# Performance work log

Measured on AMD Instinct MI355X. Metric: run time of the kernel, lower is better.

The kernel has to match this reference:

```python
import jax, jax.numpy as jnp
import numpy as np

B, T, D = 8, 2048, 256  # batch, time segments, feature dim (a_dim=v_dim=hidden=out=256)
EPS = 1e-8


def _layer_norm(x, g, b, eps=1e-6):
    m = jnp.mean(x, axis=-1, keepdims=True)
    v = jnp.var(x, axis=-1, keepdims=True)
    return (x - m) * jax.lax.rsqrt(v + eps) * g + b


def setup_inputs() -> dict:
    key = jax.random.key(0)
    ks = jax.random.split(key, 9)
    xav = lambda k: jax.random.uniform(k, (D, D), jnp.float32, -1.0, 1.0) * np.sqrt(6.0 / (D + D))
    return {
        "a_fea": jax.random.normal(ks[0], (B, T, D), jnp.float32),
        "v_fea": jax.random.normal(ks[1], (B, T, D), jnp.float32),
        "thr_val": jnp.float32(0.099),
        "Wv1": xav(ks[2]), "Wv2": xav(ks[3]), "Wvfc": xav(ks[4]),
        "Wa1": xav(ks[5]), "Wa2": xav(ks[6]), "Wafc": xav(ks[7]),
        "ln_g": jnp.ones((D,), jnp.float32),
        "ln_b": jnp.zeros((D,), jnp.float32),
    }


def reference(a_fea, v_fea, thr_val, Wv1, Wv2, Wvfc, Wa1, Wa2, Wafc, ln_g, ln_b):
    relu = jax.nn.relu
    # branch projections (dropout is identity at eval); torch Linear: x @ W.T
    v1 = relu(jnp.einsum('btd,hd->bth', v_fea, Wv1))
    v2 = relu(jnp.einsum('btd,hd->bth', v_fea, Wv2))
    a1 = relu(jnp.einsum('btd,hd->bth', a_fea, Wa1))
    a2 = relu(jnp.einsum('btd,hd->bth', a_fea, Wa2))

    d = v2.shape[-1]
    # scaled cross-modal scores, ReLU'd  [B, Tv, Ta]
    beta_va = relu(jnp.einsum('btd,bsd->bts', v2, a1) / jnp.sqrt(jnp.float32(d)))
    # a->v scores taken BEFORE row-normalization of beta_va (as in torch code)
    beta_av = jnp.transpose(beta_va, (0, 2, 1))

    time = beta_va.shape[-1]
    thr = thr_val * 10.0 / time

    # normalize -> threshold sparsify -> renormalize (v attends to a)
    bn_va = beta_va / (jnp.sum(beta_va, axis=-1, keepdims=True) + EPS)
    g_va = jnp.where(bn_va > thr, bn_va, 0.0)
    g_va = g_va / (jnp.sum(g_va, axis=-1, keepdims=True) + EPS)

    # same for a attends to v
    bn_av = beta_av / (jnp.sum(beta_av, axis=-1, keepdims=True) + EPS)
    g_av = jnp.where(bn_av > thr, bn_av, 0.0)
    g_av = g_av / (jnp.sum(g_av, axis=-1, keepdims=True) + EPS)

    # vectorized form of the diagonal selection double-loop (batch element 0)
    pred = (jnp.diagonal(g_av[0]) > 0).astype(jnp.float32)  # [T]

    a_pos = jnp.einsum('bts,bsd->btd', g_va, a2)
    v_psp = v_fea + a_pos
    v_pos = jnp.einsum('bts,bsd->btd', g_av, v1)
    a_psp = a_fea + v_pos

    v_psp = _layer_norm(relu(jnp.einsum('btd,od->bto', v_psp, Wvfc)), ln_g, ln_b)
    a_psp = _layer_norm(relu(jnp.einsum('btd,od->bto', a_psp, Wafc)), ln_g, ln_b)
    a_v_fuse = 0.5 * (v_psp + a_psp)
    return a_v_fuse, v_psp, a_psp, pred
```

## Files before the change

kernel.cpp:

```cpp
#include <hip/hip_runtime.h>
#include <math.h>

#define TT 2048
#define DD 256
#define NBATCH 8
#define EPSF 1e-8f

typedef unsigned short u16;
typedef __attribute__((ext_vector_type(8))) short short8;
typedef __attribute__((ext_vector_type(4))) float f32x4;

__device__ __forceinline__ u16 f2bf(float x) {
    unsigned int u = __builtin_bit_cast(unsigned int, x);
    u += 0x7fffu + ((u >> 16) & 1u);
    return (u16)(u >> 16);
}
__device__ __forceinline__ float bf2f(u16 h) {
    return __builtin_bit_cast(float, (unsigned int)h << 16);
}

__device__ __forceinline__ int frag_dst(int row, int k) {
    return (((row >> 4) * 4 + (k >> 3)) * 16 + (row & 15)) * 8 + (k & 7);
}

__device__ __forceinline__ int swz(int i) { return i ^ ((i >> 2) & 32); }

template<int BR>
__device__ __forceinline__ void stage_tile(const u16* __restrict__ g, u16* s,
                                           int row0, int k0, int ldk, int tid)
{
    #pragma unroll
    for (int i = 0; i < BR / 64; ++i) {
        const int c = tid + 256 * i;
        const int row = c >> 2, q = c & 3;
        *(int4*)(s + swz(frag_dst(row, q * 8))) =
            *(const int4*)(g + (long)(row0 + row) * ldk + k0 + q * 8);
    }
}

__global__ __launch_bounds__(256)
void proj_kernel(const u16* __restrict__ vfh, const u16* __restrict__ vfl,
                 const u16* __restrict__ afh, const u16* __restrict__ afl,
                 const u16* __restrict__ Wsp,
                 u16* __restrict__ v2h, u16* __restrict__ v2l,
                 u16* __restrict__ a1h, u16* __restrict__ a1l,
                 u16* __restrict__ v1T, u16* __restrict__ a2T)
{
    const int zz = blockIdx.z;
    const u16* Ah = (zz == 1 || zz == 3) ? afh : vfh;
    const u16* Al = (zz == 1 || zz == 3) ? afl : vfl;
    const int widx = (zz == 0) ? 2 : (zz == 1) ? 4 : (zz == 2) ? 0 : 6;
    const u16* Bh = Wsp + widx * DD * DD;
    const u16* Bl = Bh + DD * DD;
    const bool split = zz < 2;
    u16* Oh = (zz == 0) ? v2h : a1h;
    u16* Ol = (zz == 0) ? v2l : a1l;
    u16* OT = (zz == 2) ? v1T : a2T;

    __shared__ __align__(16) u16 Ah_s[64 * 32], Al_s[64 * 32];
    __shared__ __align__(16) u16 Bh_s[64 * 32], Bl_s[64 * 32];
    const int m0 = blockIdx.y * 64, n0 = blockIdx.x * 64;
    const int tid = threadIdx.x, lane = tid & 63, w = tid >> 6;
    const int wy = w >> 1, wx = w & 1;
    f32x4 acc[2][2] = {};

    for (int k0 = 0; k0 < DD; k0 += 32) {
        stage_tile<64>(Ah, Ah_s, m0, k0, DD, tid);
        stage_tile<64>(Al, Al_s, m0, k0, DD, tid);
        stage_tile<64>(Bh, Bh_s, n0, k0, DD, tid);
        stage_tile<64>(Bl, Bl_s, n0, k0, DD, tid);
        __syncthreads();
        short8 ah[2], al[2], bh[2], bl[2];
        #pragma unroll
        for (int i = 0; i < 2; ++i) {
            ah[i] = *(const short8*)(Ah_s + swz(((wy * 2 + i) * 64 + lane) * 8));
            al[i] = *(const short8*)(Al_s + swz(((wy * 2 + i) * 64 + lane) * 8));
        }
        #pragma unroll
        for (int j = 0; j < 2; ++j) {
            bh[j] = *(const short8*)(Bh_s + swz(((wx * 2 + j) * 64 + lane) * 8));
            bl[j] = *(const short8*)(Bl_s + swz(((wx * 2 + j) * 64 + lane) * 8));
        }
        #pragma unroll
        for (int i = 0; i < 2; ++i)
            #pragma unroll
            for (int j = 0; j < 2; ++j) {
                acc[i][j] = __builtin_amdgcn_mfma_f32_16x16x32_bf16(ah[i], bl[j], acc[i][j], 0, 0, 0);
                acc[i][j] = __builtin_amdgcn_mfma_f32_16x16x32_bf16(al[i], bh[j], acc[i][j], 0, 0, 0);
                acc[i][j] = __builtin_amdgcn_mfma_f32_16x16x32_bf16(ah[i], bh[j], acc[i][j], 0, 0, 0);
            }
        __syncthreads();
    }
    const int quad = lane >> 4, col = lane & 15;
    #pragma unroll
    for (int i = 0; i < 2; ++i)
        #pragma unroll
        for (int j = 0; j < 2; ++j) {
            const int c = n0 + (wx * 2 + j) * 16 + col;
            const int rbase = m0 + (wy * 2 + i) * 16 + quad * 4;
            if (split) {
                #pragma unroll
                for (int r = 0; r < 4; ++r) {
                    const float v = fmaxf(acc[i][j][r], 0.f);
                    const u16 h = f2bf(v);
                    Oh[(long)(rbase + r) * DD + c] = h;
                    Ol[(long)(rbase + r) * DD + c] = f2bf(v - bf2f(h));
                }
            } else {
                short4 pk;
                pk.x = (short)f2bf(fmaxf(acc[i][j][0], 0.f));
                pk.y = (short)f2bf(fmaxf(acc[i][j][1], 0.f));
                pk.z = (short)f2bf(fmaxf(acc[i][j][2], 0.f));
                pk.w = (short)f2bf(fmaxf(acc[i][j][3], 0.f));
                const int b = rbase >> 11, t = rbase & (TT - 1);
                *(short4*)(OT + ((long)b * DD + c) * TT + t) = pk;
            }
        }
}

__global__ __launch_bounds__(256)
void score_kernel(const u16* __restrict__ v2h, const u16* __restrict__ v2l,
                  const u16* __restrict__ a1h, const u16* __restrict__ a1l,
                  u16* __restrict__ beta, u16* __restrict__ betaT,
                  float* __restrict__ rs, float* __restrict__ cs)
{
    __shared__ __align__(16) u16 S[128 * 136];
    u16* Ah_s = S;
    u16* Al_s = S + 4096;
    u16* Bh_s = S + 8192;
    u16* Bl_s = S + 12288;
    const int z = blockIdx.z;
    const int m0 = blockIdx.y * 128, n0 = blockIdx.x * 128;
    const int tid = threadIdx.x, lane = tid & 63, w = tid >> 6;
    const int wy = w >> 1, wx = w & 1;
    const long zoff = (long)z * TT * DD;
    f32x4 acc[4][4] = {};

    const int prow = tid >> 2, pq = tid & 3;
    const int d0 = swz(frag_dst(prow, pq * 8));
    const int d1 = swz(frag_dst(prow + 64, pq * 8));
    const u16* gAh = v2h + zoff + (long)(m0 + prow) * DD + pq * 8;
    const u16* gAl = v2l + zoff + (long)(m0 + prow) * DD + pq * 8;
    const u16* gBh = a1h + zoff + (long)(n0 + prow) * DD + pq * 8;
    const u16* gBl = a1l + zoff + (long)(n0 + prow) * DD + pq * 8;
    const int rstep = 64 * DD;

    int4 rAh0 = *(const int4*)(gAh), rAh1 = *(const int4*)(gAh + rstep);
    int4 rAl0 = *(const int4*)(gAl), rAl1 = *(const int4*)(gAl + rstep);
    int4 rBh0 = *(const int4*)(gBh), rBh1 = *(const int4*)(gBh + rstep);
    int4 rBl0 = *(const int4*)(gBl), rBl1 = *(const int4*)(gBl + rstep);

    for (int k0 = 0; k0 < DD; k0 += 32) {
        *(int4*)(Ah_s + d0) = rAh0; *(int4*)(Ah_s + d1) = rAh1;
        *(int4*)(Al_s + d0) = rAl0; *(int4*)(Al_s + d1) = rAl1;
        *(int4*)(Bh_s + d0) = rBh0; *(int4*)(Bh_s + d1) = rBh1;
        *(int4*)(Bl_s + d0) = rBl0; *(int4*)(Bl_s + d1) = rBl1;
        __syncthreads();
        const int kn = (k0 + 32 < DD) ? k0 + 32 : 0;
        rAh0 = *(const int4*)(gAh + kn); rAh1 = *(const int4*)(gAh + rstep + kn);
        rAl0 = *(const int4*)(gAl + kn); rAl1 = *(const int4*)(gAl + rstep + kn);
        rBh0 = *(const int4*)(gBh + kn); rBh1 = *(const int4*)(gBh + rstep + kn);
        rBl0 = *(const int4*)(gBl + kn); rBl1 = *(const int4*)(gBl + rstep + kn);
        short8 ah[4], al[4], bh[4], bl[4];
        #pragma unroll
        for (int i = 0; i < 4; ++i) {
            ah[i] = *(const short8*)(Ah_s + swz(((wy * 4 + i) * 64 + lane) * 8));
            al[i] = *(const short8*)(Al_s + swz(((wy * 4 + i) * 64 + lane) * 8));
        }
        #pragma unroll
        for (int j = 0; j < 4; ++j) {
            bh[j] = *(const short8*)(Bh_s + swz(((wx * 4 + j) * 64 + lane) * 8));
            bl[j] = *(const short8*)(Bl_s + swz(((wx * 4 + j) * 64 + lane) * 8));
        }
        #pragma unroll
        for (int i = 0; i < 4; ++i)
            #pragma unroll
            for (int j = 0; j < 4; ++j) {
                acc[i][j] = __builtin_amdgcn_mfma_f32_16x16x32_bf16(ah[i], bl[j], acc[i][j], 0, 0, 0);
                acc[i][j] = __builtin_amdgcn_mfma_f32_16x16x32_bf16(al[i], bh[j], acc[i][j], 0, 0, 0);
                acc[i][j] = __builtin_amdgcn_mfma_f32_16x16x32_bf16(ah[i], bh[j], acc[i][j], 0, 0, 0);
            }
        __syncthreads();
    }

    const int quad = lane >> 4, col = lane & 15;
    const float scale = 1.f / 16.f;
    #pragma unroll
    for (int i = 0; i < 4; ++i)
        #pragma unroll
        for (int j = 0; j < 4; ++j)
            #pragma unroll
            for (int r = 0; r < 4; ++r)
                acc[i][j][r] = fmaxf(acc[i][j][r] * scale, 0.f);

    #pragma unroll
    for (int i = 0; i < 4; ++i) {
        const int rl = (wy * 4 + i) * 16 + quad * 4;
        #pragma unroll
        for (int j = 0; j < 4; ++j) {
            const int cl = (wx * 4 + j) * 16 + col;
            #pragma unroll
            for (int r = 0; r < 4; ++r)
                S[(rl + r) * 136 + cl] = f2bf(acc[i][j][r]);
        }
    }
    __syncthreads();
    #pragma unroll
    for (int it = 0; it < 8; ++it) {
        const int idx = tid + 256 * it;
        const int rl = idx >> 4, cq = idx & 15;
        const int4 v = *(const int4*)(S + rl * 136 + cq * 8);
        *(int4*)(beta + ((long)z * TT + m0 + rl) * TT + n0 + cq * 8) = v;
    }
    #pragma unroll
    for (int i = 0; i < 4; ++i)
        #pragma unroll
        for (int r = 0; r < 4; ++r) {
            float rp = 0.f;
            #pragma unroll
            for (int j = 0; j < 4; ++j) rp += acc[i][j][r];
            rp += __shfl_xor(rp, 1); rp += __shfl_xor(rp, 2);
            rp += __shfl_xor(rp, 4); rp += __shfl_xor(rp, 8);
            if (col == 0) {
                const int row = m0 + (wy * 4 + i) * 16 + quad * 4 + r;
                atomicAdd(&rs[(long)z * TT + row], rp);
            }
        }
    #pragma unroll
    for (int j = 0; j < 4; ++j) {
        float cp = 0.f;
        #pragma unroll
        for (int i = 0; i < 4; ++i)
            #pragma unroll
            for (int r = 0; r < 4; ++r) cp += acc[i][j][r];
        cp += __shfl_xor(cp, 16); cp += __shfl_xor(cp, 32);
        if (lane < 16) {
            const int c = n0 + (wx * 4 + j) * 16 + col;
            atomicAdd(&cs[(long)z * TT + c], cp);
        }
    }
    __syncthreads();
    #pragma unroll
    for (int i = 0; i < 4; ++i)
        #pragma unroll
        for (int j = 0; j < 4; ++j) {
            const int cl = (wx * 4 + j) * 16 + col;
            const int rl = (wy * 4 + i) * 16 + quad * 4;
            short4 pk;
            pk.x = (short)f2bf(acc[i][j][0]);
            pk.y = (short)f2bf(acc[i][j][1]);
            pk.z = (short)f2bf(acc[i][j][2]);
            pk.w = (short)f2bf(acc[i][j][3]);
            *(short4*)(S + cl * 136 + rl) = pk;
        }
    __syncthreads();
    #pragma unroll
    for (int it = 0; it < 8; ++it) {
        const int idx = tid + 256 * it;
        const int cl = idx >> 4, tq = idx & 15;
        const int4 v = *(const int4*)(S + cl * 136 + tq * 8);
        *(int4*)(betaT + ((long)z * TT + n0 + cl) * TT + m0 + tq * 8) = v;
    }
}

__global__ __launch_bounds__(512)
void pv_kernel(const u16* __restrict__ beta, const u16* __restrict__ betaT,
               const u16* __restrict__ a2T, const u16* __restrict__ v1T,
               const float* __restrict__ rs, const float* __restrict__ cs,
               const float* __restrict__ thrp,
               const float* __restrict__ v_fea, const float* __restrict__ a_fea,
               u16* __restrict__ yvin, u16* __restrict__ yain)
{
    __shared__ __align__(16) u16 A_s[128 * 32], B_s[256 * 32];
    __shared__ float sthr[128], sA[128], ssum[128];
    const int zz = blockIdx.x;
    const int m0 = blockIdx.y * 128;
    const int z = zz & 7;
    const bool av = zz >= 8;
    const u16* P      = av ? betaT : beta;
    const u16* VT     = av ? v1T : a2T;
    const float* sums = av ? cs : rs;
    const float* resid = av ? a_fea : v_fea;
    u16* outb         = av ? yain : yvin;

    const int tid = threadIdx.x, lane = tid & 63, w = tid >> 6;
    const int wy = w >> 2, wx = w & 3;
    const float thr = thrp[0] * 10.0f / (float)TT;
    if (tid < 128) {
        const float s = sums[(long)z * TT + m0 + tid];
        sA[tid] = s; sthr[tid] = thr * (s + EPSF); ssum[tid] = 0.f;
    }
    __syncthreads();
    f32x4 acc[4][4] = {};
    float rpart = 0.f;
    const int arow = tid >> 2, aq = tid & 3;
    const u16* Pp = P + ((long)z * TT + m0 + arow) * TT + aq * 8;
    const u16* V0 = VT + (long)z * DD * TT + (long)arow * TT + aq * 8;
    const u16* V1 = V0 + (long)128 * TT;
    const int da  = swz(frag_dst(arow, aq * 8));
    const int db1 = swz(frag_dst(arow + 128, aq * 8));

    int4 Ar  = *(const int4*)(Pp);
    int4 Br0 = *(const int4*)(V0);
    int4 Br1 = *(const int4*)(V1);

    for (int k0 = 0; k0 < TT; k0 += 32) {
        union { int4 v; u16 us[8]; } U;
        U.v = Ar;
        const float ct = sthr[arow];
        float ss = 0.f;
        #pragma unroll
        for (int t = 0; t < 8; ++t) {
            const float v = bf2f(U.us[t]);
            if (v > ct) ss += v; else U.us[t] = 0;
        }
        rpart += ss;
        *(int4*)(A_s + da) = U.v;
        *(int4*)(B_s + da) = Br0;
        *(int4*)(B_s + db1) = Br1;
        __syncthreads();
        const int kn = (k0 + 32 < TT) ? (k0 + 32) : k0;
        Ar  = *(const int4*)(Pp + kn);
        Br0 = *(const int4*)(V0 + kn);
        Br1 = *(const int4*)(V1 + kn);
        short8 a[4], b[4];
        #pragma unroll
        for (int i = 0; i < 4; ++i)
            a[i] = *(const short8*)(A_s + swz(((wy * 4 + i) * 64 + lane) * 8));
        #pragma unroll
        for (int j = 0; j < 4; ++j)
            b[j] = *(const short8*)(B_s + swz(((wx * 4 + j) * 64 + lane) * 8));
        #pragma unroll
        for (int i = 0; i < 4; ++i)
            #pragma unroll
            for (int j = 0; j < 4; ++j)
                acc[i][j] = __builtin_amdgcn_mfma_f32_16x16x32_bf16(a[i], b[j], acc[i][j], 0, 0, 0);
        __syncthreads();
    }
    atomicAdd(&ssum[arow], rpart);
    __syncthreads();

    const int quad = lane >> 4, col = lane & 15;
    #pragma unroll
    for (int i = 0; i < 4; ++i)
        #pragma unroll
        for (int j = 0; j < 4; ++j) {
            const int c = (wx * 4 + j) * 16 + col;
            #pragma unroll
            for (int r = 0; r < 4; ++r) {
                const int lrow = (wy * 4 + i) * 16 + quad * 4 + r;
                const int row = m0 + lrow;
                const float inv = 1.0f / (ssum[lrow] + EPSF * (sA[lrow] + EPSF));
                const float v = acc[i][j][r] * inv + resid[((long)z * TT + row) * DD + c];
                outb[((long)z * TT + row) * DD + c] = f2bf(v);
            }
        }
}

__global__ __launch_bounds__(256)
void fc_kernel(const u16* __restrict__ Ain, const u16* __restrict__ Wb,
               float* __restrict__ Cf)
{
    const int z = blockIdx.z;
    const u16* A = Ain + (size_t)z * (size_t)NBATCH * TT * DD;
    const u16* B = Wb + (size_t)z * DD * DD;
    float* C = Cf + (size_t)z * (size_t)NBATCH * TT * DD;
    __shared__ __align__(16) u16 A_s[128 * 32], B_s[64 * 32];
    const int m0 = blockIdx.y * 128, n0 = blockIdx.x * 64;
    const int tid = threadIdx.x, lane = tid & 63, w = tid >> 6;
    const int wy = w >> 1, wx = w & 1;
    f32x4 acc[4][2] = {};
    for (int k0 = 0; k0 < DD; k0 += 32) {
        stage_tile<128>(A, A_s, m0, k0, DD, tid);
        stage_tile<64>(B, B_s, n0, k0, DD, tid);
        __syncthreads();
        short8 a[4], b[2];
        #pragma unroll
        for (int i = 0; i < 4; ++i)
            a[i] = *(const short8*)(A_s + swz(((wy * 4 + i) * 64 + lane) * 8));
        #pragma unroll
        for (int j = 0; j < 2; ++j)
            b[j] = *(const short8*)(B_s + swz(((wx * 2 + j) * 64 + lane) * 8));
        #pragma unroll
        for (int i = 0; i < 4; ++i)
            #pragma unroll
            for (int j = 0; j < 2; ++j)
                acc[i][j] = __builtin_amdgcn_mfma_f32_16x16x32_bf16(a[i], b[j], acc[i][j], 0, 0, 0);
        __syncthreads();
    }
    const int quad = lane >> 4, col = lane & 15;
    #pragma unroll
    for (int i = 0; i < 4; ++i)
        #pragma unroll
        for (int j = 0; j < 2; ++j) {
            const int c = n0 + (wx * 2 + j) * 16 + col;
            #pragma unroll
            for (int r = 0; r < 4; ++r) {
                const int row = m0 + (wy * 4 + i) * 16 + quad * 4 + r;
                C[(long)row * DD + c] = fmaxf(acc[i][j][r], 0.f);
            }
        }
}

__global__ __launch_bounds__(256)
void pred_exact(const float* __restrict__ vf, const float* __restrict__ af,
                const float* __restrict__ Wv2, const float* __restrict__ Wa1,
                const float* __restrict__ cs, const float* __restrict__ thrp,
                float* __restrict__ pred)
{
    __shared__ float vs[8][260];
    __shared__ float as_[8][260];
    __shared__ float red[4][8];
    const int t0 = blockIdx.x * 8;
    const int tid = threadIdx.x;
    {
        const int i = tid >> 5, c = (tid & 31) * 8;
        *(float4*)&vs[i][c] = *(const float4*)(vf + (long)(t0 + i) * DD + c);
        *(float4*)&vs[i][c + 4] = *(const float4*)(vf + (long)(t0 + i) * DD + c + 4);
        *(float4*)&as_[i][c] = *(const float4*)(af + (long)(t0 + i) * DD + c);
        *(float4*)&as_[i][c + 4] = *(const float4*)(af + (long)(t0 + i) * DD + c + 4);
    }
    __syncthreads();
    const int j = tid;
    float av[8] = {0.f}, aa[8] = {0.f};
    for (int k = 0; k < DD; k += 4) {
        const float4 wv = *(const float4*)(Wv2 + (long)j * DD + k);
        const float4 wa = *(const float4*)(Wa1 + (long)j * DD + k);
        #pragma unroll
        for (int i = 0; i < 8; ++i) {
            const float4 x = *(const float4*)&vs[i][k];
            av[i] += wv.x * x.x + wv.y * x.y + wv.z * x.z + wv.w * x.w;
            const float4 y = *(const float4*)&as_[i][k];
            aa[i] += wa.x * y.x + wa.y * y.y + wa.z * y.z + wa.w * y.w;
        }
    }
    float p[8];
    #pragma unroll
    for (int i = 0; i < 8; ++i)
        p[i] = fmaxf(av[i], 0.f) * fmaxf(aa[i], 0.f);
    #pragma unroll
    for (int off = 32; off > 0; off >>= 1)
        #pragma unroll
        for (int i = 0; i < 8; ++i) p[i] += __shfl_xor(p[i], off);
    const int lane = tid & 63, wv_ = tid >> 6;
    if (lane == 0)
        #pragma unroll
        for (int i = 0; i < 8; ++i) red[wv_][i] = p[i];
    __syncthreads();
    if (tid < 8) {
        float d = red[0][tid] + red[1][tid] + red[2][tid] + red[3][tid];
        d = fmaxf(d * (1.f / 16.f), 0.f);
        const float thr = thrp[0] * 10.0f / (float)TT;
        pred[t0 + tid] = (d > thr * (cs[t0 + tid] + EPSF)) ? 1.0f : 0.0f;
    }
}

__global__ __launch_bounds__(256)
void split_feat(const float* __restrict__ vf, const float* __restrict__ af,
                u16* __restrict__ vfh, u16* __restrict__ vfl,
                u16* __restrict__ afh, u16* __restrict__ afl)
{
    const long i4 = ((long)blockIdx.x * 256 + threadIdx.x) * 4;
    const float* src = blockIdx.y ? af : vf;
    u16* dh = blockIdx.y ? afh : vfh;
    u16* dl = blockIdx.y ? afl : vfl;
    float4 a = *(const float4*)(src + i4);
    ushort4 h4, l4; u16 h;
    h = f2bf(a.x); h4.x = h; l4.x = f2bf(a.x - bf2f(h));
    h = f2bf(a.y); h4.y = h; l4.y = f2bf(a.y - bf2f(h));
    h = f2bf(a.z); h4.z = h; l4.z = f2bf(a.z - bf2f(h));
    h = f2bf(a.w); h4.w = h; l4.w = f2bf(a.w - bf2f(h));
    *(ushort4*)(dh + i4) = h4;
    *(ushort4*)(dl + i4) = l4;
}

__global__ __launch_bounds__(256)
void split_w(const float* __restrict__ w0, const float* __restrict__ w1,
             const float* __restrict__ w2, const float* __restrict__ w3,
             const float* __restrict__ w4, const float* __restrict__ w5,
             u16* __restrict__ out)
{
    const int t = blockIdx.y;
    const float* w = (t == 0) ? w0 : (t == 1) ? w1 : (t == 2) ? w2
                   : (t == 3) ? w3 : (t == 4) ? w4 : w5;
    const int i4 = (blockIdx.x * 256 + threadIdx.x) * 4;
    float4 a = *(const float4*)(w + i4);
    if (t < 4) {
        u16* oh = out + (size_t)t * 2 * DD * DD;
        u16* ol = oh + DD * DD;
        ushort4 h4, l4; u16 h;
        h = f2bf(a.x); h4.x = h; l4.x = f2bf(a.x - bf2f(h));
        h = f2bf(a.y); h4.y = h; l4.y = f2bf(a.y - bf2f(h));
        h = f2bf(a.z); h4.z = h; l4.z = f2bf(a.z - bf2f(h));
        h = f2bf(a.w); h4.w = h; l4.w = f2bf(a.w - bf2f(h));
        *(ushort4*)(oh + i4) = h4;
        *(ushort4*)(ol + i4) = l4;
    } else {
        u16* ob = out + (size_t)8 * DD * DD + (size_t)(t - 4) * DD * DD;
        ushort4 o;
        o.x = f2bf(a.x); o.y = f2bf(a.y); o.z = f2bf(a.z); o.w = f2bf(a.w);
        *(ushort4*)(ob + i4) = o;
    }
}

__global__ __launch_bounds__(256)
void ln_fuse_kernel(const float* __restrict__ yv, const float* __restrict__ ya,
                    const float* __restrict__ g, const float* __restrict__ b,
                    float* __restrict__ fuse, float* __restrict__ vpsp,
                    float* __restrict__ apsp)
{
    const long row = (long)blockIdx.x * 4 + (threadIdx.x >> 6);
    const int lane = threadIdx.x & 63;
    const float4 xv = *(const float4*)(yv + row * DD + lane * 4);
    const float4 xa = *(const float4*)(ya + row * DD + lane * 4);
    float sv = xv.x + xv.y + xv.z + xv.w;
    float sa = xa.x + xa.y + xa.z + xa.w;
    #pragma unroll
    for (int off = 32; off > 0; off >>= 1) {
        sv += __shfl_xor(sv, off);
        sa += __shfl_xor(sa, off);
    }
    const float mv = sv * (1.f / 256.f);
    const float ma = sa * (1.f / 256.f);
    const float dv0 = xv.x - mv, dv1 = xv.y - mv, dv2 = xv.z - mv, dv3 = xv.w - mv;
    const float da0 = xa.x - ma, da1 = xa.y - ma, da2 = xa.z - ma, da3 = xa.w - ma;
    float qv = dv0 * dv0 + dv1 * dv1 + dv2 * dv2 + dv3 * dv3;
    float qa = da0 * da0 + da1 * da1 + da2 * da2 + da3 * da3;
    #pragma unroll
    for (int off = 32; off > 0; off >>= 1) {
        qv += __shfl_xor(qv, off);
        qa += __shfl_xor(qa, off);
    }
    const float rv = rsqrtf(qv * (1.f / 256.f) + 1e-6f);
    const float ra = rsqrtf(qa * (1.f / 256.f) + 1e-6f);
    const float4 gg = *(const float4*)(g + lane * 4);
    const float4 bb = *(const float4*)(b + lane * 4);
    float4 ov, oa, of;
    ov.x = dv0 * rv * gg.x + bb.x; ov.y = dv1 * rv * gg.y + bb.y;
    ov.z = dv2 * rv * gg.z + bb.z; ov.w = dv3 * rv * gg.w + bb.w;
    oa.x = da0 * ra * gg.x + bb.x; oa.y = da1 * ra * gg.y + bb.y;
    oa.z = da2 * ra * gg.z + bb.z; oa.w = da3 * ra * gg.w + bb.w;
    of.x = 0.5f * (ov.x + oa.x); of.y = 0.5f * (ov.y + oa.y);
    of.z = 0.5f * (ov.z + oa.z); of.w = 0.5f * (ov.w + oa.w);
    *(float4*)(vpsp + row * DD + lane * 4) = ov;
    *(float4*)(apsp + row * DD + lane * 4) = oa;
    *(float4*)(fuse + row * DD + lane * 4) = of;
}

extern "C" void kernel_launch(void* const* d_in, const int* in_sizes, int n_in,
                              void* d_out, int out_size, void* d_ws, size_t ws_size,
                              hipStream_t stream)
{
    const float* a_fea = (const float*)d_in[0];
    const float* v_fea = (const float*)d_in[1];
    const float* thrp  = (const float*)d_in[2];
    const float* Wv1   = (const float*)d_in[3];
    const float* Wv2   = (const float*)d_in[4];
    const float* Wvfc  = (const float*)d_in[5];
    const float* Wa1   = (const float*)d_in[6];
    const float* Wa2   = (const float*)d_in[7];
    const float* Wafc  = (const float*)d_in[8];
    const float* lng   = (const float*)d_in[9];
    const float* lnb   = (const float*)d_in[10];

    const long MT = (long)NBATCH * TT;
    float* out_fuse = (float*)d_out;
    float* out_vpsp = out_fuse + MT * DD;
    float* out_apsp = out_vpsp + MT * DD;
    float* out_pred = out_apsp + MT * DD;

    char* ws = (char*)d_ws;
    const size_t fb = (size_t)MT * DD * sizeof(u16);
    const size_t sumB = (size_t)MT * sizeof(float);
    u16* v2h  = (u16*)(ws + 0 * fb);
    u16* v2l  = (u16*)(ws + 1 * fb);
    u16* a1h  = (u16*)(ws + 2 * fb);
    u16* a1l  = (u16*)(ws + 3 * fb);
    u16* yvin = (u16*)(ws + 4 * fb);
    u16* yain = (u16*)(ws + 5 * fb);
    u16* v1T  = (u16*)(ws + 6 * fb);
    u16* a2T  = (u16*)(ws + 7 * fb);
    char* p = ws + 8 * fb;
    float* rs = (float*)(p + 0 * sumB);
    float* cs = (float*)(p + 1 * sumB);
    u16* Wsp  = (u16*)(p + 2 * sumB);
    char* q = p + 2 * sumB + 10 * DD * DD * sizeof(u16);
    const size_t betaB = (size_t)NBATCH * TT * TT * sizeof(u16);
    u16* beta  = (u16*)q;
    u16* betaT = (u16*)(q + betaB);
    u16* vfh = (u16*)q;
    u16* vfl = vfh + MT * DD;
    u16* afh = vfl + MT * DD;
    u16* afl = afh + MT * DD;
    float* yv = (float*)(ws + 0 * fb);
    float* ya = (float*)(ws + 2 * fb);

    hipMemsetAsync(rs, 0, 2 * sumB, stream);

    const dim3 blk(256, 1, 1);

    split_feat<<<dim3((unsigned)(MT * DD / 1024), 2, 1), blk, 0, stream>>>(
        v_fea, a_fea, vfh, vfl, afh, afl);
    split_w<<<dim3(DD * DD / 1024, 6, 1), blk, 0, stream>>>(
        Wv1, Wv2, Wa1, Wa2, Wvfc, Wafc, Wsp);

    proj_kernel<<<dim3(DD / 64, (unsigned)(MT / 64), 4), blk, 0, stream>>>(
        vfh, vfl, afh, afl, Wsp, v2h, v2l, a1h, a1l, v1T, a2T);

    score_kernel<<<dim3(TT / 128, TT / 128, NBATCH), blk, 0, stream>>>(
        v2h, v2l, a1h, a1l, beta, betaT, rs, cs);
    pred_exact<<<dim3(TT / 8, 1, 1), blk, 0, stream>>>(
        v_fea, a_fea, Wv2, Wa1, cs, thrp, out_pred);

    pv_kernel<<<dim3(2 * NBATCH, TT / 128, 1), dim3(512, 1, 1), 0, stream>>>(
        beta, betaT, a2T, v1T, rs, cs, thrp, v_fea, a_fea, yvin, yain);

    fc_kernel<<<dim3(DD / 64, (unsigned)(MT / 128), 2), blk, 0, stream>>>(
        yvin, Wsp + 8 * DD * DD, yv);
    ln_fuse_kernel<<<dim3((unsigned)(MT / 4), 1, 1), blk, 0, stream>>>(
        yv, ya, lng, lnb, out_fuse, out_vpsp, out_apsp);
}
```

Before: 430.2 us.

## Use 512-thread score blocks and store FC outputs as bf16

The score kernel moves from 256 to 512 threads per block with a 2x4 wave layout. Each wave now holds a 4x2 accumulator tile instead of 4x4, and each thread loads one global vector per operand instead of two. This cuts register pressure per thread and adds more waves to hide latency, at the cost of more LDS traffic per MFMA. Separately, the FC kernel writes its ReLU output as bf16 rather than fp32, halving intermediate traffic into the layernorm kernel but adding rounding error before the normalization.

```diff
diff --git a/kernel.cpp b/kernel.cpp
--- a/kernel.cpp
+++ b/kernel.cpp
@@ -118,7 +118,7 @@
         }
 }
 
-__global__ __launch_bounds__(256)
+__global__ __launch_bounds__(512)
 void score_kernel(const u16* __restrict__ v2h, const u16* __restrict__ v2l,
                   const u16* __restrict__ a1h, const u16* __restrict__ a1l,
                   u16* __restrict__ beta, u16* __restrict__ betaT,
@@ -132,50 +132,48 @@
     const int z = blockIdx.z;
     const int m0 = blockIdx.y * 128, n0 = blockIdx.x * 128;
     const int tid = threadIdx.x, lane = tid & 63, w = tid >> 6;
-    const int wy = w >> 1, wx = w & 1;
+    const int wy = w >> 2, wx = w & 3;
     const long zoff = (long)z * TT * DD;
-    f32x4 acc[4][4] = {};
+    f32x4 acc[4][2] = {};
 
     const int prow = tid >> 2, pq = tid & 3;
     const int d0 = swz(frag_dst(prow, pq * 8));
-    const int d1 = swz(frag_dst(prow + 64, pq * 8));
     const u16* gAh = v2h + zoff + (long)(m0 + prow) * DD + pq * 8;
     const u16* gAl = v2l + zoff + (long)(m0 + prow) * DD + pq * 8;
     const u16* gBh = a1h + zoff + (long)(n0 + prow) * DD + pq * 8;
     const u16* gBl = a1l + zoff + (long)(n0 + prow) * DD + pq * 8;
-    const int rstep = 64 * DD;
-
-    int4 rAh0 = *(const int4*)(gAh), rAh1 = *(const int4*)(gAh + rstep);
-    int4 rAl0 = *(const int4*)(gAl), rAl1 = *(const int4*)(gAl + rstep);
-    int4 rBh0 = *(const int4*)(gBh), rBh1 = *(const int4*)(gBh + rstep);
-    int4 rBl0 = *(const int4*)(gBl), rBl1 = *(const int4*)(gBl + rstep);
+
+    int4 rAh = *(const int4*)(gAh);
+    int4 rAl = *(const int4*)(gAl);
+    int4 rBh = *(const int4*)(gBh);
+    int4 rBl = *(const int4*)(gBl);
 
     for (int k0 = 0; k0 < DD; k0 += 32) {
-        *(int4*)(Ah_s + d0) = rAh0; *(int4*)(Ah_s + d1) = rAh1;
-        *(int4*)(Al_s + d0) = rAl0; *(int4*)(Al_s + d1) = rAl1;
-        *(int4*)(Bh_s + d0) = rBh0; *(int4*)(Bh_s + d1) = rBh1;
-        *(int4*)(Bl_s + d0) = rBl0; *(int4*)(Bl_s + d1) = rBl1;
+        *(int4*)(Ah_s + d0) = rAh;
+        *(int4*)(Al_s + d0) = rAl;
+        *(int4*)(Bh_s + d0) = rBh;
+        *(int4*)(Bl_s + d0) = rBl;
         __syncthreads();
         const int kn = (k0 + 32 < DD) ? k0 + 32 : 0;
-        rAh0 = *(const int4*)(gAh + kn); rAh1 = *(const int4*)(gAh + rstep + kn);
-        rAl0 = *(const int4*)(gAl + kn); rAl1 = *(const int4*)(gAl + rstep + kn);
-        rBh0 = *(const int4*)(gBh + kn); rBh1 = *(const int4*)(gBh + rstep + kn);
-        rBl0 = *(const int4*)(gBl + kn); rBl1 = *(const int4*)(gBl + rstep + kn);
-        short8 ah[4], al[4], bh[4], bl[4];
+        rAh = *(const int4*)(gAh + kn);
+        rAl = *(const int4*)(gAl + kn);
+        rBh = *(const int4*)(gBh + kn);
+        rBl = *(const int4*)(gBl + kn);
+        short8 ah[4], al[4], bh[2], bl[2];
         #pragma unroll
         for (int i = 0; i < 4; ++i) {
             ah[i] = *(const short8*)(Ah_s + swz(((wy * 4 + i) * 64 + lane) * 8));
             al[i] = *(const short8*)(Al_s + swz(((wy * 4 + i) * 64 + lane) * 8));
         }
         #pragma unroll
-        for (int j = 0; j < 4; ++j) {
-            bh[j] = *(const short8*)(Bh_s + swz(((wx * 4 + j) * 64 + lane) * 8));
-            bl[j] = *(const short8*)(Bl_s + swz(((wx * 4 + j) * 64 + lane) * 8));
+        for (int j = 0; j < 2; ++j) {
+            bh[j] = *(const short8*)(Bh_s + swz(((wx * 2 + j) * 64 + lane) * 8));
+            bl[j] = *(const short8*)(Bl_s + swz(((wx * 2 + j) * 64 + lane) * 8));
         }
         #pragma unroll
         for (int i = 0; i < 4; ++i)
             #pragma unroll
-            for (int j = 0; j < 4; ++j) {
+            for (int j = 0; j < 2; ++j) {
                 acc[i][j] = __builtin_amdgcn_mfma_f32_16x16x32_bf16(ah[i], bl[j], acc[i][j], 0, 0, 0);
                 acc[i][j] = __builtin_amdgcn_mfma_f32_16x16x32_bf16(al[i], bh[j], acc[i][j], 0, 0, 0);
                 acc[i][j] = __builtin_amdgcn_mfma_f32_16x16x32_bf16(ah[i], bh[j], acc[i][j], 0, 0, 0);
@@ -188,7 +186,7 @@
     #pragma unroll
     for (int i = 0; i < 4; ++i)
         #pragma unroll
-        for (int j = 0; j < 4; ++j)
+        for (int j = 0; j < 2; ++j)
             #pragma unroll
             for (int r = 0; r < 4; ++r)
                 acc[i][j][r] = fmaxf(acc[i][j][r] * scale, 0.f);
@@ -197,8 +195,8 @@
     for (int i = 0; i < 4; ++i) {
         const int rl = (wy * 4 + i) * 16 + quad * 4;
         #pragma unroll
-        for (int j = 0; j < 4; ++j) {
-            const int cl = (wx * 4 + j) * 16 + col;
+        for (int j = 0; j < 2; ++j) {
+            const int cl = (wx * 2 + j) * 16 + col;
             #pragma unroll
             for (int r = 0; r < 4; ++r)
                 S[(rl + r) * 136 + cl] = f2bf(acc[i][j][r]);
@@ -206,8 +204,8 @@
     }
     __syncthreads();
     #pragma unroll
-    for (int it = 0; it < 8; ++it) {
-        const int idx = tid + 256 * it;
+    for (int it = 0; it < 4; ++it) {
+        const int idx = tid + 512 * it;
         const int rl = idx >> 4, cq = idx & 15;
         const int4 v = *(const int4*)(S + rl * 136 + cq * 8);
         *(int4*)(beta + ((long)z * TT + m0 + rl) * TT + n0 + cq * 8) = v;
@@ -216,9 +214,7 @@
     for (int i = 0; i < 4; ++i)
         #pragma unroll
         for (int r = 0; r < 4; ++r) {
-            float rp = 0.f;
-            #pragma unroll
-            for (int j = 0; j < 4; ++j) rp += acc[i][j][r];
+            float rp = acc[i][0][r] + acc[i][1][r];
             rp += __shfl_xor(rp, 1); rp += __shfl_xor(rp, 2);
             rp += __shfl_xor(rp, 4); rp += __shfl_xor(rp, 8);
             if (col == 0) {
@@ -227,7 +223,7 @@
             }
         }
     #pragma unroll
-    for (int j = 0; j < 4; ++j) {
+    for (int j = 0; j < 2; ++j) {
         float cp = 0.f;
         #pragma unroll
         for (int i = 0; i < 4; ++i)
@@ -235,7 +231,7 @@
             for (int r = 0; r < 4; ++r) cp += acc[i][j][r];
         cp += __shfl_xor(cp, 16); cp += __shfl_xor(cp, 32);
         if (lane < 16) {
-            const int c = n0 + (wx * 4 + j) * 16 + col;
+            const int c = n0 + (wx * 2 + j) * 16 + col;
             atomicAdd(&cs[(long)z * TT + c], cp);
         }
     }
@@ -243,8 +239,8 @@
     #pragma unroll
     for (int i = 0; i < 4; ++i)
         #pragma unroll
-        for (int j = 0; j < 4; ++j) {
-            const int cl = (wx * 4 + j) * 16 + col;
+        for (int j = 0; j < 2; ++j) {
+            const int cl = (wx * 2 + j) * 16 + col;
             const int rl = (wy * 4 + i) * 16 + quad * 4;
             short4 pk;
             pk.x = (short)f2bf(acc[i][j][0]);
@@ -255,8 +251,8 @@
         }
     __syncthreads();
     #pragma unroll
-    for (int it = 0; it < 8; ++it) {
-        const int idx = tid + 256 * it;
+    for (int it = 0; it < 4; ++it) {
+        const int idx = tid + 512 * it;
         const int cl = idx >> 4, tq = idx & 15;
         const int4 v = *(const int4*)(S + cl * 136 + tq * 8);
         *(int4*)(betaT + ((long)z * TT + n0 + cl) * TT + m0 + tq * 8) = v;
@@ -359,12 +355,12 @@
 
 __global__ __launch_bounds__(256)
 void fc_kernel(const u16* __restrict__ Ain, const u16* __restrict__ Wb,
-               float* __restrict__ Cf)
+               u16* __restrict__ Cb)
 {
     const int z = blockIdx.z;
     const u16* A = Ain + (size_t)z * (size_t)NBATCH * TT * DD;
     const u16* B = Wb + (size_t)z * DD * DD;
-    float* C = Cf + (size_t)z * (size_t)NBATCH * TT * DD;
+    u16* C = Cb + (size_t)z * (size_t)NBATCH * TT * DD;
     __shared__ __align__(16) u16 A_s[128 * 32], B_s[64 * 32];
     const int m0 = blockIdx.y * 128, n0 = blockIdx.x * 64;
     const int tid = threadIdx.x, lane = tid & 63, w = tid >> 6;
@@ -397,7 +393,7 @@
             #pragma unroll
             for (int r = 0; r < 4; ++r) {
                 const int row = m0 + (wy * 4 + i) * 16 + quad * 4 + r;
-                C[(long)row * DD + c] = fmaxf(acc[i][j][r], 0.f);
+                C[(long)row * DD + c] = f2bf(fmaxf(acc[i][j][r], 0.f));
             }
         }
 }
@@ -504,17 +500,19 @@
 }
 
 __global__ __launch_bounds__(256)
-void ln_fuse_kernel(const float* __restrict__ yv, const float* __restrict__ ya,
+void ln_fuse_kernel(const u16* __restrict__ yv, const u16* __restrict__ ya,
                     const float* __restrict__ g, const float* __restrict__ b,
                     float* __restrict__ fuse, float* __restrict__ vpsp,
                     float* __restrict__ apsp)
 {
     const long row = (long)blockIdx.x * 4 + (threadIdx.x >> 6);
     const int lane = threadIdx.x & 63;
-    const float4 xv = *(const float4*)(yv + row * DD + lane * 4);
-    const float4 xa = *(const float4*)(ya + row * DD + lane * 4);
-    float sv = xv.x + xv.y + xv.z + xv.w;
-    float sa = xa.x + xa.y + xa.z + xa.w;
+    const ushort4 hv = *(const ushort4*)(yv + row * DD + lane * 4);
+    const ushort4 ha = *(const ushort4*)(ya + row * DD + lane * 4);
+    const float xv0 = bf2f(hv.x), xv1 = bf2f(hv.y), xv2 = bf2f(hv.z), xv3 = bf2f(hv.w);
+    const float xa0 = bf2f(ha.x), xa1 = bf2f(ha.y), xa2 = bf2f(ha.z), xa3 = bf2f(ha.w);
+    float sv = xv0 + xv1 + xv2 + xv3;
+    float sa = xa0 + xa1 + xa2 + xa3;
     #pragma unroll
     for (int off = 32; off > 0; off >>= 1) {
         sv += __shfl_xor(sv, off);
@@ -522,8 +520,8 @@
     }
     const float mv = sv * (1.f / 256.f);
     const float ma = sa * (1.f / 256.f);
-    const float dv0 = xv.x - mv, dv1 = xv.y - mv, dv2 = xv.z - mv, dv3 = xv.w - mv;
-    const float da0 = xa.x - ma, da1 = xa.y - ma, da2 = xa.z - ma, da3 = xa.w - ma;
+    const float dv0 = xv0 - mv, dv1 = xv1 - mv, dv2 = xv2 - mv, dv3 = xv3 - mv;
+    const float da0 = xa0 - ma, da1 = xa1 - ma, da2 = xa2 - ma, da3 = xa3 - ma;
     float qv = dv0 * dv0 + dv1 * dv1 + dv2 * dv2 + dv3 * dv3;
     float qa = da0 * da0 + da1 * da1 + da2 * da2 + da3 * da3;
     #pragma unroll
@@ -592,8 +590,8 @@
     u16* vfl = vfh + MT * DD;
     u16* afh = vfl + MT * DD;
     u16* afl = afh + MT * DD;
-    float* yv = (float*)(ws + 0 * fb);
-    float* ya = (float*)(ws + 2 * fb);
+    u16* yvb = (u16*)(ws + 0 * fb);
+    u16* yab = yvb + (size_t)MT * DD;
 
     hipMemsetAsync(rs, 0, 2 * sumB, stream);
 
@@ -607,7 +605,7 @@
     proj_kernel<<<dim3(DD / 64, (unsigned)(MT / 64), 4), blk, 0, stream>>>(
         vfh, vfl, afh, afl, Wsp, v2h, v2l, a1h, a1l, v1T, a2T);
 
-    score_kernel<<<dim3(TT / 128, TT / 128, NBATCH), blk, 0, stream>>>(
+    score_kernel<<<dim3(TT / 128, TT / 128, NBATCH), dim3(512, 1, 1), 0, stream>>>(
         v2h, v2l, a1h, a1l, beta, betaT, rs, cs);
     pred_exact<<<dim3(TT / 8, 1, 1), blk, 0, stream>>>(
         v_fea, a_fea, Wv2, Wa1, cs, thrp, out_pred);
@@ -616,7 +614,7 @@
         beta, betaT, a2T, v1T, rs, cs, thrp, v_fea, a_fea, yvin, yain);
 
     fc_kernel<<<dim3(DD / 64, (unsigned)(MT / 128), 2), blk, 0, stream>>>(
-        yvin, Wsp + 8 * DD * DD, yv);
+        yvin, Wsp + 8 * DD * DD, yvb);
     ln_fuse_kernel<<<dim3((unsigned)(MT / 4), 1, 1), blk, 0, stream>>>(
-        yv, ya, lng, lnb, out_fuse, out_vpsp, out_apsp);
-}
+        yvb, yab, lng, lnb, out_fuse, out_vpsp, out_apsp);
+}
```

New measurement: 402.4 us. 6.5% less time.
